# Kernel tuning notes

Measured on AMD Instinct MI355X. Metric: run time of the kernel, lower is better.

Reference implementation:

```python
import jax, jax.numpy as jnp
import numpy as np

NUM_Q = 8      # num_quantizers
K = 1024       # codebook_size (num_tokens)
D = 512        # feature dim
B, T = 16, 2000
BETA = 0.25    # commitment weight


def setup_inputs() -> dict:
    key = jax.random.key(0)
    kx, kc = jax.random.split(key)
    x = jax.random.normal(kx, (B, T, D), dtype=jnp.float32)
    # learned codebooks, one per quantizer stage: [NUM_Q, K, D]
    codebooks = jax.random.normal(kc, (NUM_Q, K, D), dtype=jnp.float32)
    return {"x": x, "codebooks": codebooks}


def _vq_stage(residual, codebook):
    """Single VQ layer: nearest-codeword search + straight-through + commitment loss.
    residual: [B, T, D]; codebook: [K, D]."""
    sg = jax.lax.stop_gradient
    # squared L2 distances via ||r||^2 - 2 r.e + ||e||^2  -> [B, T, K]
    r2 = jnp.sum(residual * residual, axis=-1, keepdims=True)          # [B,T,1]
    e2 = jnp.sum(codebook * codebook, axis=-1)                          # [K]
    dots = jnp.einsum('btd,kd->btk', residual, codebook)                # [B,T,K]
    dist = r2 - 2.0 * dots + e2
    indices = jnp.argmin(dist, axis=-1)                                 # [B,T] int
    quantized = codebook[indices]                                       # [B,T,D] gather
    # commitment + codebook loss (VQ-VAE style)
    loss = (BETA * jnp.mean((sg(quantized) - residual) ** 2)
            + jnp.mean((quantized - sg(residual)) ** 2))
    # straight-through estimator
    quantized_st = residual + sg(quantized - residual)
    return quantized_st, indices, loss


def reference(x, codebooks):
    def step(carry, codebook):
        residual, q_out = carry
        q, idx, loss = _vq_stage(residual, codebook)
        residual = residual - jax.lax.stop_gradient(q)
        return (residual, q_out + q), (idx, loss)

    init = (x, jnp.zeros_like(x))
    (_, quantized_out), (all_indices, all_losses) = jax.lax.scan(step, init, codebooks)
    # all_indices: [NUM_Q, B, T]; mean loss across stages
    return quantized_out, all_indices, jnp.mean(all_losses)
```

## Files before the change

### kernel.cpp

```cpp
#include <hip/hip_runtime.h>

#define M_TOK 32000
#define DIM   512
#define KCB   1024
#define NQ    8
#define BM 256

typedef _Float16 f16x8 __attribute__((ext_vector_type(8)));
typedef _Float16 f16x4 __attribute__((ext_vector_type(4)));
typedef float f32x4 __attribute__((ext_vector_type(4)));

#define SBAR() __builtin_amdgcn_s_barrier()
#define SFENCE() __builtin_amdgcn_sched_barrier(0)
#define WAIT_VM(N) asm volatile("s_waitcnt vmcnt(" #N ")" ::: "memory")

__device__ __forceinline__ void gload_lds16(const void* g, void* l) {
  __builtin_amdgcn_global_load_lds(
      (const __attribute__((address_space(1))) unsigned int*)g,
      (__attribute__((address_space(3))) unsigned int*)l, 16, 0, 0);
}

__device__ __forceinline__ float wave_reduce_sum(float v) {
#pragma unroll
  for (int off = 32; off > 0; off >>= 1) v += __shfl_xor(v, off, 64);
  return v;
}

__device__ __forceinline__ unsigned int fenc(float f) {
  unsigned int u = __float_as_uint(f);
  return (u & 0x80000000u) ? ~u : (u | 0x80000000u);
}

__device__ __forceinline__ _Float16 hi16(float v) { return (_Float16)v; }
__device__ __forceinline__ _Float16 lo16(float v, _Float16 h) {
  return (_Float16)(v - (float)h);
}

struct Split4 { f16x4 h, l; };
__device__ __forceinline__ Split4 split4(float4 v) {
  Split4 s;
  s.h[0] = hi16(v.x); s.l[0] = lo16(v.x, s.h[0]);
  s.h[1] = hi16(v.y); s.l[1] = lo16(v.y, s.h[1]);
  s.h[2] = hi16(v.z); s.l[2] = lo16(v.z, s.h[2]);
  s.h[3] = hi16(v.w); s.l[3] = lo16(v.w, s.h[3]);
  return s;
}

__global__ __launch_bounds__(256) void rvq_init_kernel(
    const float* __restrict__ x, const float* __restrict__ cb,
    float* __restrict__ e2, float* __restrict__ r2,
    unsigned long long* __restrict__ keys, float* __restrict__ lossCell,
    _Float16* __restrict__ ahi, _Float16* __restrict__ alo) {
  if (blockIdx.x == 0 && threadIdx.x == 0) *lossCell = 0.f;
  for (int i = blockIdx.x * 256 + threadIdx.x; i < M_TOK; i += gridDim.x * 256)
    keys[i] = ~0ull;
  int row = blockIdx.x * 4 + (threadIdx.x >> 6);
  int lane = threadIdx.x & 63;
  if (row < NQ * KCB) {
    const float4* s4 = (const float4*)(cb + (size_t)row * DIM);
    float s = 0.f;
    float4 v = s4[lane];
    s += v.x * v.x + v.y * v.y + v.z * v.z + v.w * v.w;
    v = s4[lane + 64];
    s += v.x * v.x + v.y * v.y + v.z * v.z + v.w * v.w;
    s = wave_reduce_sum(s);
    if (lane == 0) e2[row] = s;
  } else {
    int t = row - NQ * KCB;
    if (t >= M_TOK) return;
    const float4* s4 = (const float4*)(x + (size_t)t * DIM);
    float4 v0 = s4[lane], v1 = s4[lane + 64];
    float s = v0.x * v0.x + v0.y * v0.y + v0.z * v0.z + v0.w * v0.w
            + v1.x * v1.x + v1.y * v1.y + v1.z * v1.z + v1.w * v1.w;
    Split4 s0 = split4(v0), s1 = split4(v1);
    size_t base = (size_t)t * DIM + lane * 4;
    *(f16x4*)(ahi + base) = s0.h;
    *(f16x4*)(alo + base) = s0.l;
    *(f16x4*)(ahi + base + 256) = s1.h;
    *(f16x4*)(alo + base + 256) = s1.l;
    s = wave_reduce_sum(s);
    if (lane == 0) r2[t] = s;
  }
}

__global__ __launch_bounds__(256) void rvq_split_cb_kernel(
    const float* __restrict__ cb, _Float16* __restrict__ cbF) {
  int gid = blockIdx.x * 256 + threadIdx.x;
  int c = gid & 1023;
  int nc = (gid >> 10) & 3;
  int bt = (gid >> 12) & 31;
  int s = gid >> 17;
  if (s >= NQ) return;
  int col = nc * 256 + (c >> 6) * 16 + (c & 15);
  int k = (bt & 15) * 32 + ((c >> 4) & 3) * 8;
  const float* src = cb + ((size_t)s * KCB + col) * DIM + k;
  int isLo = bt >> 4;
  f16x8 out;
#pragma unroll
  for (int j = 0; j < 8; ++j) {
    _Float16 h = hi16(src[j]);
    out[j] = isLo ? lo16(src[j], h) : h;
  }
  *(f16x8*)(cbF + (size_t)gid * 8) = out;
}

__global__ __launch_bounds__(512, 1) void rvq_argmin_kernel(
    const _Float16* __restrict__ ahi,
    const _Float16* __restrict__ alo,
    const _Float16* __restrict__ cbF,
    const float* __restrict__ e2,
    const float* __restrict__ r2,
    unsigned long long* __restrict__ keys) {
  __shared__ _Float16 bufA[2][2][8192];
  __shared__ _Float16 bufB[2][2][8192];

  const int tid = threadIdx.x;
  const int lane = tid & 63, w = tid >> 6;
  const int l15 = lane & 15, l4 = lane >> 4;
  const int wr = w >> 2, wc = w & 3;

  const int bid = blockIdx.x;
  const int xcd = bid & 7, org = bid >> 3;
  const int wg = ((xcd < 4) ? xcd * 63 : 252 + (xcd - 4) * 62) + org;
  const int m0 = (wg >> 2) * BM;
  const int nc = wg & 3;

  const int q0 = tid, q1 = tid + 512;
  const size_t aoff0 = (size_t)(m0 + ((q0 >> 6) << 4) + (q0 & 15)) * DIM + ((q0 >> 4) & 3) * 8;
  const size_t aoff1 = (size_t)(m0 + ((q1 >> 6) << 4) + (q1 & 15)) * DIM + ((q1 >> 4) & 3) * 8;

  auto stageTile = [&](int j, int buf) {
    const int ko = j * 32;
    gload_lds16(ahi + aoff0 + ko, &bufA[buf][0][(size_t)q0 * 8]);
    gload_lds16(ahi + aoff1 + ko, &bufA[buf][0][(size_t)q1 * 8]);
    gload_lds16(alo + aoff0 + ko, &bufA[buf][1][(size_t)q0 * 8]);
    gload_lds16(alo + aoff1 + ko, &bufA[buf][1][(size_t)q1 * 8]);
    const _Float16* bh = cbF + (size_t)(j * 4 + nc) * 8192;
    const _Float16* bl = cbF + (size_t)((16 + j) * 4 + nc) * 8192;
    gload_lds16(bh + (size_t)q0 * 8, &bufB[buf][0][(size_t)q0 * 8]);
    gload_lds16(bh + (size_t)q1 * 8, &bufB[buf][0][(size_t)q1 * 8]);
    gload_lds16(bl + (size_t)q0 * 8, &bufB[buf][1][(size_t)q0 * 8]);
    gload_lds16(bl + (size_t)q1 * 8, &bufB[buf][1][(size_t)q1 * 8]);
  };

  f32x4 acc[8][4];
#pragma unroll
  for (int a = 0; a < 8; ++a)
#pragma unroll
    for (int b = 0; b < 4; ++b) acc[a][b] = (f32x4){0.f, 0.f, 0.f, 0.f};

  stageTile(0, 0);
  for (int j = 0; j < 16; ++j) {
    const int cur = j & 1;
    if (j < 15) {
      stageTile(j + 1, cur ^ 1);
      SFENCE();
      WAIT_VM(8);
    } else {
      SFENCE();
      WAIT_VM(0);
    }
    SFENCE();
    SBAR();
    SFENCE();
    const _Float16* Ah = bufA[cur][0];
    const _Float16* Al = bufA[cur][1];
    const _Float16* Bh = bufB[cur][0];
    const _Float16* Bl = bufB[cur][1];
    f16x8 ah[8], al[8];
#pragma unroll
    for (int mf = 0; mf < 8; ++mf) {
      ah[mf] = *(const f16x8*)(Ah + (size_t)((wr * 8 + mf) * 64 + lane) * 8);
      al[mf] = *(const f16x8*)(Al + (size_t)((wr * 8 + mf) * 64 + lane) * 8);
    }
    __builtin_amdgcn_s_setprio(1);
#pragma unroll
    for (int nf = 0; nf < 4; ++nf) {
      f16x8 bh = *(const f16x8*)(Bh + (size_t)((wc * 4 + nf) * 64 + lane) * 8);
      f16x8 bl = *(const f16x8*)(Bl + (size_t)((wc * 4 + nf) * 64 + lane) * 8);
#pragma unroll
      for (int mf = 0; mf < 8; ++mf)
        acc[mf][nf] = __builtin_amdgcn_mfma_f32_16x16x32_f16(ah[mf], bh, acc[mf][nf], 0, 0, 0);
#pragma unroll
      for (int mf = 0; mf < 8; ++mf)
        acc[mf][nf] = __builtin_amdgcn_mfma_f32_16x16x32_f16(ah[mf], bl, acc[mf][nf], 0, 0, 0);
#pragma unroll
      for (int mf = 0; mf < 8; ++mf)
        acc[mf][nf] = __builtin_amdgcn_mfma_f32_16x16x32_f16(al[mf], bh, acc[mf][nf], 0, 0, 0);
    }
    __builtin_amdgcn_s_setprio(0);
    SFENCE();
    SBAR();
  }

  const int colbase = nc * 256 + wc * 64;
  float minv[32];
  int mini[32];
#pragma unroll
  for (int i = 0; i < 32; ++i) { minv[i] = 3.4e38f; mini[i] = 0; }
#pragma unroll
  for (int nf = 0; nf < 4; ++nf) {
    int colg = colbase + nf * 16 + l15;
    float e2v = e2[colg];
#pragma unroll
    for (int mf = 0; mf < 8; ++mf) {
      float4 rv = *(const float4*)(r2 + m0 + wr * 128 + mf * 16 + l4 * 4);
      float rva[4] = {rv.x, rv.y, rv.z, rv.w};
#pragma unroll
      for (int rr = 0; rr < 4; ++rr) {
        float d = (rva[rr] - 2.f * acc[mf][nf][rr]) + e2v;
        int ii = mf * 4 + rr;
        if (d < minv[ii]) { minv[ii] = d; mini[ii] = colg; }
      }
    }
  }
#pragma unroll
  for (int mf = 0; mf < 8; ++mf) {
#pragma unroll
    for (int rr = 0; rr < 4; ++rr) {
      int ii = mf * 4 + rr;
      float v = minv[ii];
      int ix = mini[ii];
#pragma unroll
      for (int off = 8; off; off >>= 1) {
        float ov = __shfl_xor(v, off, 16);
        int oi = __shfl_xor(ix, off, 16);
        if (ov < v || (ov == v && oi < ix)) { v = ov; ix = oi; }
      }
      if (l15 == 0) {
        int tok = m0 + wr * 128 + mf * 16 + l4 * 4 + rr;
        unsigned long long key = ((unsigned long long)fenc(v) << 32) | (unsigned)ix;
        atomicMin(&keys[tok], key);
      }
    }
  }
}

__global__ __launch_bounds__(256) void rvq_update_kernel(
    const float* __restrict__ rin, const float* __restrict__ cb,
    unsigned long long* __restrict__ keys,
    float* __restrict__ rout, float* __restrict__ r2out,
    float* __restrict__ idx_out, float* __restrict__ lossCell,
    _Float16* __restrict__ ahi, _Float16* __restrict__ alo) {
  const int wave = threadIdx.x >> 6, lane = threadIdx.x & 63;
  __shared__ float lred[4];
  float lpart = 0.f;
  for (int r = wave; r < 64; r += 4) {
    const int tok = blockIdx.x * 64 + r;
    const unsigned idx = (unsigned)(keys[tok] & 0xffffffffu);
    const float4* rrow = (const float4*)(rin + (size_t)tok * DIM);
    const float4* crow = (const float4*)(cb + (size_t)idx * DIM);
    float4* orow = (float4*)(rout + (size_t)tok * DIM);
    float ssq_t = 0.f, ssq_r = 0.f;
#pragma unroll
    for (int c4 = 0; c4 < 2; ++c4) {
      int c = lane + c4 * 64;
      float4 a = rrow[c], q = crow[c];
      float4 t = make_float4(q.x - a.x, q.y - a.y, q.z - a.z, q.w - a.w);
      float4 qst = make_float4(a.x + t.x, a.y + t.y, a.z + t.z, a.w + t.w);
      float4 rn = make_float4(a.x - qst.x, a.y - qst.y, a.z - qst.z, a.w - qst.w);
      orow[c] = rn;
      Split4 sp = split4(rn);
      *(f16x4*)(ahi + (size_t)tok * DIM + c * 4) = sp.h;
      *(f16x4*)(alo + (size_t)tok * DIM + c * 4) = sp.l;
      ssq_t += t.x * t.x + t.y * t.y + t.z * t.z + t.w * t.w;
      ssq_r += rn.x * rn.x + rn.y * rn.y + rn.z * rn.z + rn.w * rn.w;
    }
    float tot_t = wave_reduce_sum(ssq_t);
    float tot_r = wave_reduce_sum(ssq_r);
    if (lane == 0) {
      idx_out[tok] = (float)idx;
      keys[tok] = ~0ull;
      r2out[tok] = tot_r;
      lpart += tot_t;
    }
  }
  if (lane == 0) lred[wave] = lpart;
  __syncthreads();
  if (threadIdx.x == 0)
    atomicAdd(lossCell, lred[0] + lred[1] + lred[2] + lred[3]);
}

__global__ __launch_bounds__(256) void rvq_finalize_kernel(
    const float* __restrict__ x, float* __restrict__ out,
    const float* __restrict__ lossCell, float* __restrict__ loss_out) {
  size_t i = (size_t)blockIdx.x * 256 + threadIdx.x;
  const size_t n4 = (size_t)M_TOK * DIM / 4;
  if (i < n4) {
    const float4* x4 = (const float4*)x;
    float4* o4 = (float4*)out;
    float4 a = x4[i], r = o4[i];
    o4[i] = make_float4(a.x - r.x, a.y - r.y, a.z - r.z, a.w - r.w);
  }
  if (blockIdx.x == 0 && threadIdx.x == 0) {
    *loss_out = *lossCell * (1.25f / 131072000.f);
  }
}

extern "C" void kernel_launch(void* const* d_in, const int* in_sizes, int n_in,
                              void* d_out, int out_size, void* d_ws, size_t ws_size,
                              hipStream_t stream) {
  const float* x = (const float*)d_in[0];
  const float* cb = (const float*)d_in[1];
  float* out = (float*)d_out;
  float* idx_out = out + (size_t)M_TOK * DIM;
  float* loss_out = idx_out + (size_t)NQ * M_TOK;

  char* wsp = (char*)d_ws;
  unsigned long long* keys = (unsigned long long*)wsp;
  float* e2 = (float*)(wsp + 262144);
  float* r2 = (float*)(wsp + 294912);
  float* lossCell = (float*)(wsp + 425984);
  _Float16* cbF = (_Float16*)(wsp + 524288);
  _Float16* ahi = (_Float16*)(wsp + 524288 + 16777216);
  _Float16* alo = ahi + (size_t)M_TOK * DIM;

  {
    int rows = NQ * KCB + M_TOK;
    rvq_init_kernel<<<(rows + 3) / 4, 256, 0, stream>>>(x, cb, e2, r2, keys,
                                                        lossCell, ahi, alo);
    rvq_split_cb_kernel<<<(NQ << 17) / 256, 256, 0, stream>>>(cb, cbF);
  }
  float* resbuf = out;
  const size_t stageF = (size_t)1 << 20;
  for (int s = 0; s < NQ; ++s) {
    const float* rin = (s == 0) ? x : resbuf;
    rvq_argmin_kernel<<<(M_TOK / BM) * 4, 512, 0, stream>>>(
        ahi, alo, cbF + (size_t)s * stageF, e2 + s * KCB, r2, keys);
    rvq_update_kernel<<<M_TOK / 64, 256, 0, stream>>>(
        rin, cb + (size_t)s * KCB * DIM, keys, resbuf, r2,
        idx_out + (size_t)s * M_TOK, lossCell, ahi, alo);
  }
  rvq_finalize_kernel<<<(M_TOK * DIM / 4 + 255) / 256, 256, 0, stream>>>(
      x, out, lossCell, loss_out);
}
```

Baseline: 1.222 ms.

## Switch argmin GEMM to 32x32x16 MFMA with row-major split codebook layout

```diff
diff --git a/kernel.cpp b/kernel.cpp
--- a/kernel.cpp
+++ b/kernel.cpp
@@ -8,7 +8,7 @@
 
 typedef _Float16 f16x8 __attribute__((ext_vector_type(8)));
 typedef _Float16 f16x4 __attribute__((ext_vector_type(4)));
-typedef float f32x4 __attribute__((ext_vector_type(4)));
+typedef float f32x16 __attribute__((ext_vector_type(16)));
 
 #define SBAR() __builtin_amdgcn_s_barrier()
 #define SFENCE() __builtin_amdgcn_sched_barrier(0)
@@ -84,39 +84,34 @@
 }
 
 __global__ __launch_bounds__(256) void rvq_split_cb_kernel(
-    const float* __restrict__ cb, _Float16* __restrict__ cbF) {
-  int gid = blockIdx.x * 256 + threadIdx.x;
-  int c = gid & 1023;
-  int nc = (gid >> 10) & 3;
-  int bt = (gid >> 12) & 31;
-  int s = gid >> 17;
-  if (s >= NQ) return;
-  int col = nc * 256 + (c >> 6) * 16 + (c & 15);
-  int k = (bt & 15) * 32 + ((c >> 4) & 3) * 8;
-  const float* src = cb + ((size_t)s * KCB + col) * DIM + k;
-  int isLo = bt >> 4;
-  f16x8 out;
-#pragma unroll
-  for (int j = 0; j < 8; ++j) {
-    _Float16 h = hi16(src[j]);
-    out[j] = isLo ? lo16(src[j], h) : h;
-  }
-  *(f16x8*)(cbF + (size_t)gid * 8) = out;
+    const float* __restrict__ cb, _Float16* __restrict__ cbh,
+    _Float16* __restrict__ cbl) {
+  size_t gid = (size_t)blockIdx.x * 256 + threadIdx.x;
+  if (gid >= (size_t)NQ * KCB * DIM / 8) return;
+  size_t base = gid * 8;
+  float4 v0 = *(const float4*)(cb + base);
+  float4 v1 = *(const float4*)(cb + base + 4);
+  Split4 s0 = split4(v0), s1 = split4(v1);
+  *(f16x4*)(cbh + base) = s0.h;
+  *(f16x4*)(cbh + base + 4) = s1.h;
+  *(f16x4*)(cbl + base) = s0.l;
+  *(f16x4*)(cbl + base + 4) = s1.l;
 }
 
 __global__ __launch_bounds__(512, 1) void rvq_argmin_kernel(
     const _Float16* __restrict__ ahi,
     const _Float16* __restrict__ alo,
-    const _Float16* __restrict__ cbF,
+    const _Float16* __restrict__ cbh,
+    const _Float16* __restrict__ cbl,
     const float* __restrict__ e2,
     const float* __restrict__ r2,
     unsigned long long* __restrict__ keys) {
-  __shared__ _Float16 bufA[2][2][8192];
-  __shared__ _Float16 bufB[2][2][8192];
+  __shared__ _Float16 As[2][16384];
+  __shared__ _Float16 Bs[2][16384];
 
   const int tid = threadIdx.x;
   const int lane = tid & 63, w = tid >> 6;
-  const int l15 = lane & 15, l4 = lane >> 4;
+  const int l31 = lane & 31, l5 = lane >> 5;
   const int wr = w >> 2, wc = w & 3;
 
   const int bid = blockIdx.x;
@@ -124,111 +119,121 @@
   const int wg = ((xcd < 4) ? xcd * 63 : 252 + (xcd - 4) * 62) + org;
   const int m0 = (wg >> 2) * BM;
   const int nc = wg & 3;
-
-  const int q0 = tid, q1 = tid + 512;
-  const size_t aoff0 = (size_t)(m0 + ((q0 >> 6) << 4) + (q0 & 15)) * DIM + ((q0 >> 4) & 3) * 8;
-  const size_t aoff1 = (size_t)(m0 + ((q1 >> 6) << 4) + (q1 & 15)) * DIM + ((q1 >> 4) & 3) * 8;
-
-  auto stageTile = [&](int j, int buf) {
-    const int ko = j * 32;
-    gload_lds16(ahi + aoff0 + ko, &bufA[buf][0][(size_t)q0 * 8]);
-    gload_lds16(ahi + aoff1 + ko, &bufA[buf][0][(size_t)q1 * 8]);
-    gload_lds16(alo + aoff0 + ko, &bufA[buf][1][(size_t)q0 * 8]);
-    gload_lds16(alo + aoff1 + ko, &bufA[buf][1][(size_t)q1 * 8]);
-    const _Float16* bh = cbF + (size_t)(j * 4 + nc) * 8192;
-    const _Float16* bl = cbF + (size_t)((16 + j) * 4 + nc) * 8192;
-    gload_lds16(bh + (size_t)q0 * 8, &bufB[buf][0][(size_t)q0 * 8]);
-    gload_lds16(bh + (size_t)q1 * 8, &bufB[buf][0][(size_t)q1 * 8]);
-    gload_lds16(bl + (size_t)q0 * 8, &bufB[buf][1][(size_t)q0 * 8]);
-    gload_lds16(bl + (size_t)q1 * 8, &bufB[buf][1][(size_t)q1 * 8]);
+  const int c0 = nc * 256;
+
+  const size_t laneoff = (size_t)l31 * DIM + l5 * 8;
+  const _Float16* pA[4];
+  const _Float16* pB[4];
+#pragma unroll
+  for (int i = 0; i < 4; ++i) {
+    int s = w * 4 + i;
+    int kh = s & 1, r = (s >> 1) & 7, p = s >> 4;
+    pA[i] = (p ? alo : ahi) + (size_t)(m0 + r * 32) * DIM + kh * 16 + laneoff;
+    pB[i] = (p ? cbl : cbh) + (size_t)(c0 + r * 32) * DIM + kh * 16 + laneoff;
+  }
+  _Float16* dA0 = &As[0][(w * 4) * 512];
+  _Float16* dA1 = &As[1][(w * 4) * 512];
+  _Float16* dB0 = &Bs[0][(w * 4) * 512];
+  _Float16* dB1 = &Bs[1][(w * 4) * 512];
+  auto stageNext = [&](int buf) {
+    _Float16* da = buf ? dA1 : dA0;
+    _Float16* db = buf ? dB1 : dB0;
+#pragma unroll
+    for (int i = 0; i < 4; ++i) {
+      gload_lds16(pA[i], da + i * 512);
+      pA[i] += 32;
+    }
+#pragma unroll
+    for (int i = 0; i < 4; ++i) {
+      gload_lds16(pB[i], db + i * 512);
+      pB[i] += 32;
+    }
   };
 
-  f32x4 acc[8][4];
-#pragma unroll
-  for (int a = 0; a < 8; ++a)
-#pragma unroll
-    for (int b = 0; b < 4; ++b) acc[a][b] = (f32x4){0.f, 0.f, 0.f, 0.f};
-
-  stageTile(0, 0);
+  const char* Ab0 = (const char*)&As[0][0] + wr * 8192 + lane * 16;
+  const char* Ab1 = (const char*)&As[1][0] + wr * 8192 + lane * 16;
+  const char* Bb0 = (const char*)&Bs[0][0] + wc * 4096 + lane * 16;
+  const char* Bb1 = (const char*)&Bs[1][0] + wc * 4096 + lane * 16;
+
+  f32x16 acc[8];
+#pragma unroll
+  for (int a = 0; a < 8; ++a) acc[a] = (f32x16)(0.f);
+
+  stageNext(0);
   for (int j = 0; j < 16; ++j) {
     const int cur = j & 1;
     if (j < 15) {
-      stageTile(j + 1, cur ^ 1);
-      SFENCE();
+      stageNext(cur ^ 1);
       WAIT_VM(8);
     } else {
-      SFENCE();
       WAIT_VM(0);
     }
-    SFENCE();
     SBAR();
     SFENCE();
-    const _Float16* Ah = bufA[cur][0];
-    const _Float16* Al = bufA[cur][1];
-    const _Float16* Bh = bufB[cur][0];
-    const _Float16* Bl = bufB[cur][1];
-    f16x8 ah[8], al[8];
-#pragma unroll
-    for (int mf = 0; mf < 8; ++mf) {
-      ah[mf] = *(const f16x8*)(Ah + (size_t)((wr * 8 + mf) * 64 + lane) * 8);
-      al[mf] = *(const f16x8*)(Al + (size_t)((wr * 8 + mf) * 64 + lane) * 8);
-    }
+    const char* Ab = cur ? Ab1 : Ab0;
+    const char* Bb = cur ? Bb1 : Bb0;
+    f16x8 b[2][2][2];
+#pragma unroll
+    for (int nf = 0; nf < 2; ++nf)
+#pragma unroll
+      for (int p = 0; p < 2; ++p)
+#pragma unroll
+        for (int kh = 0; kh < 2; ++kh)
+          b[nf][p][kh] = *(const f16x8*)(Bb + p * 16384 + nf * 2048 + kh * 1024);
     __builtin_amdgcn_s_setprio(1);
 #pragma unroll
-    for (int nf = 0; nf < 4; ++nf) {
-      f16x8 bh = *(const f16x8*)(Bh + (size_t)((wc * 4 + nf) * 64 + lane) * 8);
-      f16x8 bl = *(const f16x8*)(Bl + (size_t)((wc * 4 + nf) * 64 + lane) * 8);
-#pragma unroll
-      for (int mf = 0; mf < 8; ++mf)
-        acc[mf][nf] = __builtin_amdgcn_mfma_f32_16x16x32_f16(ah[mf], bh, acc[mf][nf], 0, 0, 0);
-#pragma unroll
-      for (int mf = 0; mf < 8; ++mf)
-        acc[mf][nf] = __builtin_amdgcn_mfma_f32_16x16x32_f16(ah[mf], bl, acc[mf][nf], 0, 0, 0);
-#pragma unroll
-      for (int mf = 0; mf < 8; ++mf)
-        acc[mf][nf] = __builtin_amdgcn_mfma_f32_16x16x32_f16(al[mf], bh, acc[mf][nf], 0, 0, 0);
+    for (int mr = 0; mr < 4; ++mr) {
+      f16x8 a[2][2];
+#pragma unroll
+      for (int p = 0; p < 2; ++p)
+#pragma unroll
+        for (int kh = 0; kh < 2; ++kh)
+          a[p][kh] = *(const f16x8*)(Ab + p * 16384 + mr * 2048 + kh * 1024);
+#pragma unroll
+      for (int nf = 0; nf < 2; ++nf) {
+        f32x16 c = acc[mr * 2 + nf];
+        c = __builtin_amdgcn_mfma_f32_32x32x16_f16(a[0][0], b[nf][0][0], c, 0, 0, 0);
+        c = __builtin_amdgcn_mfma_f32_32x32x16_f16(a[0][1], b[nf][0][1], c, 0, 0, 0);
+        c = __builtin_amdgcn_mfma_f32_32x32x16_f16(a[0][0], b[nf][1][0], c, 0, 0, 0);
+        c = __builtin_amdgcn_mfma_f32_32x32x16_f16(a[0][1], b[nf][1][1], c, 0, 0, 0);
+        c = __builtin_amdgcn_mfma_f32_32x32x16_f16(a[1][0], b[nf][0][0], c, 0, 0, 0);
+        c = __builtin_amdgcn_mfma_f32_32x32x16_f16(a[1][1], b[nf][0][1], c, 0, 0, 0);
+        acc[mr * 2 + nf] = c;
+      }
     }
     __builtin_amdgcn_s_setprio(0);
     SFENCE();
     SBAR();
   }
 
-  const int colbase = nc * 256 + wc * 64;
-  float minv[32];
-  int mini[32];
-#pragma unroll
-  for (int i = 0; i < 32; ++i) { minv[i] = 3.4e38f; mini[i] = 0; }
-#pragma unroll
-  for (int nf = 0; nf < 4; ++nf) {
-    int colg = colbase + nf * 16 + l15;
-    float e2v = e2[colg];
-#pragma unroll
-    for (int mf = 0; mf < 8; ++mf) {
-      float4 rv = *(const float4*)(r2 + m0 + wr * 128 + mf * 16 + l4 * 4);
-      float rva[4] = {rv.x, rv.y, rv.z, rv.w};
-#pragma unroll
-      for (int rr = 0; rr < 4; ++rr) {
-        float d = (rva[rr] - 2.f * acc[mf][nf][rr]) + e2v;
-        int ii = mf * 4 + rr;
-        if (d < minv[ii]) { minv[ii] = d; mini[ii] = colg; }
-      }
-    }
-  }
-#pragma unroll
-  for (int mf = 0; mf < 8; ++mf) {
-#pragma unroll
-    for (int rr = 0; rr < 4; ++rr) {
-      int ii = mf * 4 + rr;
-      float v = minv[ii];
-      int ix = mini[ii];
-#pragma unroll
-      for (int off = 8; off; off >>= 1) {
-        float ov = __shfl_xor(v, off, 16);
-        int oi = __shfl_xor(ix, off, 16);
+  const int colb = c0 + wc * 64 + l31;
+  const float e2v0 = e2[colb];
+  const float e2v1 = e2[colb + 32];
+#pragma unroll
+  for (int mr = 0; mr < 4; ++mr) {
+    const int rowb = m0 + wr * 128 + mr * 32;
+    float rv[16];
+#pragma unroll
+    for (int g = 0; g < 4; ++g) {
+      float4 q = *(const float4*)(r2 + rowb + g * 8 + l5 * 4);
+      rv[g * 4 + 0] = q.x; rv[g * 4 + 1] = q.y;
+      rv[g * 4 + 2] = q.z; rv[g * 4 + 3] = q.w;
+    }
+#pragma unroll
+    for (int reg = 0; reg < 16; ++reg) {
+      float d0 = (rv[reg] - 2.f * acc[mr * 2 + 0][reg]) + e2v0;
+      float d1 = (rv[reg] - 2.f * acc[mr * 2 + 1][reg]) + e2v1;
+      float v = d0;
+      int ix = colb;
+      if (d1 < v) { v = d1; ix = colb + 32; }
+#pragma unroll
+      for (int off = 16; off; off >>= 1) {
+        float ov = __shfl_xor(v, off, 32);
+        int oi = __shfl_xor(ix, off, 32);
         if (ov < v || (ov == v && oi < ix)) { v = ov; ix = oi; }
       }
-      if (l15 == 0) {
-        int tok = m0 + wr * 128 + mf * 16 + l4 * 4 + rr;
+      if (l31 == 0) {
+        int tok = rowb + (reg >> 2) * 8 + l5 * 4 + (reg & 3);
         unsigned long long key = ((unsigned long long)fenc(v) << 32) | (unsigned)ix;
         atomicMin(&keys[tok], key);
       }
@@ -311,7 +316,8 @@
   float* e2 = (float*)(wsp + 262144);
   float* r2 = (float*)(wsp + 294912);
   float* lossCell = (float*)(wsp + 425984);
-  _Float16* cbF = (_Float16*)(wsp + 524288);
+  _Float16* cbh = (_Float16*)(wsp + 524288);
+  _Float16* cbl = (_Float16*)(wsp + 524288 + 8388608);
   _Float16* ahi = (_Float16*)(wsp + 524288 + 16777216);
   _Float16* alo = ahi + (size_t)M_TOK * DIM;
 
@@ -319,14 +325,15 @@
     int rows = NQ * KCB + M_TOK;
     rvq_init_kernel<<<(rows + 3) / 4, 256, 0, stream>>>(x, cb, e2, r2, keys,
                                                         lossCell, ahi, alo);
-    rvq_split_cb_kernel<<<(NQ << 17) / 256, 256, 0, stream>>>(cb, cbF);
+    int n8 = NQ * KCB * DIM / 8;
+    rvq_split_cb_kernel<<<n8 / 256, 256, 0, stream>>>(cb, cbh, cbl);
   }
   float* resbuf = out;
-  const size_t stageF = (size_t)1 << 20;
   for (int s = 0; s < NQ; ++s) {
     const float* rin = (s == 0) ? x : resbuf;
     rvq_argmin_kernel<<<(M_TOK / BM) * 4, 512, 0, stream>>>(
-        ahi, alo, cbF + (size_t)s * stageF, e2 + s * KCB, r2, keys);
+        ahi, alo, cbh + (size_t)s * KCB * DIM, cbl + (size_t)s * KCB * DIM,
+        e2 + s * KCB, r2, keys);
     rvq_update_kernel<<<M_TOK / 64, 256, 0, stream>>>(
         rin, cb + (size_t)s * KCB * DIM, keys, resbuf, r2,
         idx_out + (size_t)s * M_TOK, lossCell, ahi, alo);
```

After: 1.644 ms. 34.5% more time.
